# Kernel tuning notes

Hardware: AMD Instinct MI355X
Metric: run time of the kernel (lower is better)

## Reference

```python
import jax, jax.numpy as jnp
import numpy as np

HEAD_NUM = 16

def setup_inputs() -> dict:
    key = jax.random.key(0)
    kq, kk, kv = jax.random.split(key, 3)
    shape = (4, 2048, 1024)  # [B, N, C]
    return {
        "query_layer": jax.random.normal(kq, shape, dtype=jnp.float32),
        "key_layer": jax.random.normal(kk, shape, dtype=jnp.float32),
        "value_layer": jax.random.normal(kv, shape, dtype=jnp.float32),
    }

def _split_heads(x, h):
    B, N, C = x.shape
    return x.reshape(B, N, h, C // h).transpose(0, 2, 1, 3)  # [B,H,N,d]

def reference(query_layer, key_layer, value_layer):
    B, N, C = query_layer.shape
    h = HEAD_NUM
    d = C // h
    q = _split_heads(query_layer, h)
    k = _split_heads(key_layer, h)
    v = _split_heads(value_layer, h)
    scores = jnp.einsum('bhnd,bhmd->bhnm', q, k) / jnp.sqrt(jnp.asarray(d, q.dtype))
    probs = jax.nn.softmax(scores, axis=-1)
    ctx = jnp.einsum('bhnm,bhmd->bhnd', probs, v)
    return ctx.transpose(0, 2, 1, 3).reshape(B, N, C)
```

## Files before the change

### kernel.cpp

```cpp
#include <hip/hip_runtime.h>
#include <hip/hip_bf16.h>

#define B_   4
#define N_   2048
#define C_   1024
#define NT   32
#define QSCALE 0.18033688011112042f

typedef __attribute__((ext_vector_type(8)))  short short8;
typedef __attribute__((ext_vector_type(4)))  float f32x4;
typedef __attribute__((ext_vector_type(16))) float f32x16;
typedef __attribute__((ext_vector_type(2)))  int   int2v;

__device__ __forceinline__ unsigned short f2bf(float x) {
    union { __hip_bfloat16 h; unsigned short u; } c;
    c.h = __float2bfloat16(x);
    return c.u;
}
__device__ __forceinline__ float fast_exp2(float x) {
    float r; asm("v_exp_f32 %0, %1" : "=v"(r) : "v"(x)); return r;
}
__device__ __forceinline__ int cvtpk(float a, float b) {
    int r; asm("v_cvt_pk_bf16_f32 %0, %1, %2" : "=v"(r) : "v"(a), "v"(b)); return r;
}

__global__ __launch_bounds__(256) void prepack(
    const float* __restrict__ K, const float* __restrict__ V,
    unsigned short* __restrict__ Kt, unsigned short* __restrict__ Vt)
{
    __shared__ __align__(16) unsigned short kl[4096];
    __shared__ __align__(16) unsigned short vl[4096];
    const int L = blockIdx.x;
    const int xcd = L & 7;
    const int j = L >> 3;
    const int head = xcd + 8 * (j >> 5);
    const int t = j & 31;
    const int b = head >> 4, h = head & 15;
    const int tid = threadIdx.x;
    const int r = tid >> 2, cb = tid & 3;
    const size_t head_off = (size_t)b * N_ * C_ + (size_t)h * 64;
    const int kv0 = t * 64;
    const int blk_out = head * NT + t;

    {
        const float* src = K + head_off + (size_t)(kv0 + r) * C_ + cb * 16;
        f32x4 x0 = *(const f32x4*)(src);
        f32x4 x1 = *(const f32x4*)(src + 4);
        f32x4 x2 = *(const f32x4*)(src + 8);
        f32x4 x3 = *(const f32x4*)(src + 12);
        short8 p0, p1;
        #pragma unroll
        for (int i = 0; i < 4; ++i) {
            p0[i] = (short)f2bf(x0[i]); p0[i + 4] = (short)f2bf(x1[i]);
            p1[i] = (short)f2bf(x2[i]); p1[i + 4] = (short)f2bf(x3[i]);
        }
        const int swz = (r & 7) << 3;
        *(short8*)&kl[r * 64 + ((cb * 16) ^ swz)]     = p0;
        *(short8*)&kl[r * 64 + ((cb * 16 + 8) ^ swz)] = p1;
    }
    {
        const float* src = V + head_off + (size_t)(kv0 + r) * C_ + cb * 16;
        f32x4 y0 = *(const f32x4*)(src);
        f32x4 y1 = *(const f32x4*)(src + 4);
        f32x4 y2 = *(const f32x4*)(src + 8);
        f32x4 y3 = *(const f32x4*)(src + 12);
        #pragma unroll
        for (int i = 0; i < 4; ++i) {
            int d0 = cb * 16 + i;
            vl[d0 * 64 + (r ^ ((d0 & 7) << 3))] = f2bf(y0[i]);
            int d1 = cb * 16 + 4 + i;
            vl[d1 * 64 + (r ^ ((d1 & 7) << 3))] = f2bf(y1[i]);
            int d2 = cb * 16 + 8 + i;
            vl[d2 * 64 + (r ^ ((d2 & 7) << 3))] = f2bf(y2[i]);
            int d3 = cb * 16 + 12 + i;
            vl[d3 * 64 + (r ^ ((d3 & 7) << 3))] = f2bf(y3[i]);
        }
    }
    __syncthreads();
    #pragma unroll
    for (int cc = 0; cc < 2; ++cc) {
        const int c  = tid + cc * 256;
        const int f  = c >> 6;
        const int ln = c & 63;
        const int row = (f & 1) * 32 + (ln & 31);
        const int col = (f >> 1) * 16 + (ln >> 5) * 8;
        const int sw  = (row & 7) << 3;
        short8 kk = *(const short8*)&kl[row * 64 + (col ^ sw)];
        short8 vv = *(const short8*)&vl[row * 64 + (col ^ sw)];
        *(short8*)&Kt[(size_t)blk_out * 4096 + c * 8] = kk;
        *(short8*)&Vt[(size_t)blk_out * 4096 + c * 8] = vv;
    }
}

__global__ __launch_bounds__(256, 4) void attn_fwd(
    const float* __restrict__ Q, const unsigned short* __restrict__ Kt,
    const unsigned short* __restrict__ Vt, float* __restrict__ O)
{
    __shared__ __align__(16) unsigned short klds[2][4096];

    const int L = blockIdx.x;
    const int xcd = L & 7;
    const int j = L >> 3;
    const int head = xcd + 8 * (j >> 4);
    const int qt = j & 15;
    const int b = head >> 4, h = head & 15;

    const int tid  = threadIdx.x;
    const int wave = tid >> 6;
    const int lane = tid & 63;
    const int l31  = lane & 31;
    const int hi   = lane >> 5;

    const unsigned short* kbase = Kt + (size_t)head * (NT * 4096);
    const unsigned short* vbase = Vt + (size_t)head * (NT * 4096);
    const float* qp = Q + (size_t)b * N_ * C_ + (size_t)h * 64;
    float*       op = O + (size_t)b * N_ * C_ + (size_t)h * 64;

    const int qrow = qt * 128 + wave * 32 + l31;
    short8 qfrag[4];
    {
        const float* qr = qp + (size_t)qrow * C_ + hi * 8;
        #pragma unroll
        for (int ks = 0; ks < 4; ++ks) {
            f32x4 x0 = *(const f32x4*)(qr + ks * 16);
            f32x4 x1 = *(const f32x4*)(qr + ks * 16 + 4);
            short8 a;
            #pragma unroll
            for (int i = 0; i < 4; ++i) {
                a[i]     = (short)f2bf(x0[i] * QSCALE);
                a[i + 4] = (short)f2bf(x1[i] * QSCALE);
            }
            qfrag[ks] = a;
        }
    }

    f32x16 o0 = {}, o1 = {};
    float m_r = -3.0e38f, l_r = 0.0f;

    const int lofs = lane * 8;

    auto stageK = [&](int t, int buf) {
        const unsigned short* kg = kbase + (size_t)t * 4096 + wave * 1024 + lofs;
        __builtin_amdgcn_global_load_lds((const __attribute__((address_space(1))) void*)kg,
            (__attribute__((address_space(3))) void*)&klds[buf][wave * 1024], 16, 0, 0);
        __builtin_amdgcn_global_load_lds((const __attribute__((address_space(1))) void*)(kg + 512),
            (__attribute__((address_space(3))) void*)&klds[buf][wave * 1024 + 512], 16, 0, 0);
    };

    stageK(0, 0);
    __syncthreads();
    int cur = 0;

    for (int t = 0; t < NT; ++t) {
        if (t + 1 < NT) stageK(t + 1, cur ^ 1);

        const unsigned short* vtp = vbase + (size_t)t * 4096 + lofs;
        short8 vA0 = *(const short8*)(vtp);
        short8 vA1 = *(const short8*)(vtp + 512);
        short8 vA2 = *(const short8*)(vtp + 1024);
        short8 vA3 = *(const short8*)(vtp + 1536);

        const unsigned short* kl = klds[cur];

        f32x16 s0 = {}, s1 = {};
        __builtin_amdgcn_s_setprio(1);
        #pragma unroll
        for (int ks = 0; ks < 4; ++ks) {
            short8 kf0 = *(const short8*)&kl[ks * 1024 + lofs];
            short8 kf1 = *(const short8*)&kl[ks * 1024 + 512 + lofs];
            s0 = __builtin_amdgcn_mfma_f32_32x32x16_bf16(kf0, qfrag[ks], s0, 0, 0, 0);
            s1 = __builtin_amdgcn_mfma_f32_32x32x16_bf16(kf1, qfrag[ks], s1, 0, 0, 0);
        }
        __builtin_amdgcn_s_setprio(0);

        float mx[8];
        #pragma unroll
        for (int r = 0; r < 8; ++r) mx[r] = fmaxf(fmaxf(s0[r], s0[r + 8]), fmaxf(s1[r], s1[r + 8]));
        #pragma unroll
        for (int st = 4; st; st >>= 1) {
            #pragma unroll
            for (int r = 0; r < st; ++r) mx[r] = fmaxf(mx[r], mx[r + st]);
        }
        int2v msw = __builtin_amdgcn_permlane32_swap(__float_as_int(mx[0]), __float_as_int(mx[0]), false, false);
        const float rm = fmaxf(__int_as_float(msw[0]), __int_as_float(msw[1]));

        if (!__all(rm - m_r <= 8.0f)) {
            const float mnew = fmaxf(m_r, rm);
            const float corr = fast_exp2(m_r - mnew);
            m_r = mnew;
            l_r *= corr;
            #pragma unroll
            for (int r = 0; r < 16; ++r) { o0[r] *= corr; o1[r] *= corr; }
        }

        #pragma unroll
        for (int r = 0; r < 16; ++r) {
            s0[r] = fast_exp2(s0[r] - m_r);
            s1[r] = fast_exp2(s1[r] - m_r);
        }
        float aa[8];
        #pragma unroll
        for (int r = 0; r < 8; ++r) aa[r] = (s0[r] + s0[r + 8]) + (s1[r] + s1[r + 8]);
        #pragma unroll
        for (int st = 4; st; st >>= 1) {
            #pragma unroll
            for (int r = 0; r < st; ++r) aa[r] += aa[r + st];
        }
        int2v ssw = __builtin_amdgcn_permlane32_swap(__float_as_int(aa[0]), __float_as_int(aa[0]), false, false);
        l_r += __int_as_float(ssw[0]) + __int_as_float(ssw[1]);

        short8 pf[4];
        #pragma unroll
        for (int ct = 0; ct < 2; ++ct) {
            #pragma unroll
            for (int kss = 0; kss < 2; ++kss) {
                float e0, e1, e2, e3, e4, e5, e6, e7;
                if (ct == 0) {
                    e0 = s0[8*kss+0]; e1 = s0[8*kss+1]; e2 = s0[8*kss+2]; e3 = s0[8*kss+3];
                    e4 = s0[8*kss+4]; e5 = s0[8*kss+5]; e6 = s0[8*kss+6]; e7 = s0[8*kss+7];
                } else {
                    e0 = s1[8*kss+0]; e1 = s1[8*kss+1]; e2 = s1[8*kss+2]; e3 = s1[8*kss+3];
                    e4 = s1[8*kss+4]; e5 = s1[8*kss+5]; e6 = s1[8*kss+6]; e7 = s1[8*kss+7];
                }
                int w0 = cvtpk(e0, e1);
                int w1 = cvtpk(e2, e3);
                int w2 = cvtpk(e4, e5);
                int w3 = cvtpk(e6, e7);
                int2v sA = __builtin_amdgcn_permlane32_swap(w0, w2, false, false);
                int2v sB = __builtin_amdgcn_permlane32_swap(w1, w3, false, false);
                union { int i[4]; short8 v; } u;
                u.i[0] = sA[0]; u.i[1] = sB[0]; u.i[2] = sA[1]; u.i[3] = sB[1];
                pf[ct * 2 + kss] = u.v;
            }
        }

        short8 vB0 = *(const short8*)(vtp + 2048);
        short8 vB1 = *(const short8*)(vtp + 2560);
        short8 vB2 = *(const short8*)(vtp + 3072);
        short8 vB3 = *(const short8*)(vtp + 3584);

        __builtin_amdgcn_s_setprio(1);
        o0 = __builtin_amdgcn_mfma_f32_32x32x16_bf16(vA0, pf[0], o0, 0, 0, 0);
        o1 = __builtin_amdgcn_mfma_f32_32x32x16_bf16(vA1, pf[0], o1, 0, 0, 0);
        o0 = __builtin_amdgcn_mfma_f32_32x32x16_bf16(vA2, pf[1], o0, 0, 0, 0);
        o1 = __builtin_amdgcn_mfma_f32_32x32x16_bf16(vA3, pf[1], o1, 0, 0, 0);
        o0 = __builtin_amdgcn_mfma_f32_32x32x16_bf16(vB0, pf[2], o0, 0, 0, 0);
        o1 = __builtin_amdgcn_mfma_f32_32x32x16_bf16(vB1, pf[2], o1, 0, 0, 0);
        o0 = __builtin_amdgcn_mfma_f32_32x32x16_bf16(vB2, pf[3], o0, 0, 0, 0);
        o1 = __builtin_amdgcn_mfma_f32_32x32x16_bf16(vB3, pf[3], o1, 0, 0, 0);
        __builtin_amdgcn_s_setprio(0);

        __syncthreads();
        cur ^= 1;
    }

    const float inv = 1.0f / l_r;
    float* orow = op + (size_t)qrow * C_;
    #pragma unroll
    for (int bb = 0; bb < 4; ++bb) {
        f32x4 w0, w1;
        #pragma unroll
        for (int i = 0; i < 4; ++i) {
            w0[i] = o0[4 * bb + i] * inv;
            w1[i] = o1[4 * bb + i] * inv;
        }
        *(f32x4*)(orow + 8 * bb + 4 * hi)      = w0;
        *(f32x4*)(orow + 32 + 8 * bb + 4 * hi) = w1;
    }
}

extern "C" void kernel_launch(void* const* d_in, const int* in_sizes, int n_in,
                              void* d_out, int out_size, void* d_ws, size_t ws_size,
                              hipStream_t stream) {
    const float* q = (const float*)d_in[0];
    const float* k = (const float*)d_in[1];
    const float* v = (const float*)d_in[2];
    float* o = (float*)d_out;
    unsigned short* Kt = (unsigned short*)d_ws;
    unsigned short* Vt = Kt + (size_t)64 * NT * 4096;
    prepack<<<dim3(64 * NT), dim3(256), 0, stream>>>(k, v, Kt, Vt);
    attn_fwd<<<dim3(1024), dim3(256), 0, stream>>>(q, Kt, Vt, o);
}
```

Baseline: 113.7 us.

## Software-pipeline PV MFMA of previous tile with QK MFMA of current tile

Restructures the KV loop so the P·V matrix multiplies for tile t-1 are issued right after the Q·K multiplies for tile t. This interleaves the MFMA work with the softmax exp/convert work of the next tile, and double-buffers the probability fragments across iterations. It also folds the running-max subtraction into the score accumulator's initial value. The row-sum permlane reduction is deferred to a single swap at the end. The cost is more live registers (V fragments and two P buffers), which can lower occupancy or cause spills.

```diff
diff --git a/kernel.cpp b/kernel.cpp
--- a/kernel.cpp
+++ b/kernel.cpp
@@ -135,7 +135,7 @@
     }
 
     f32x16 o0 = {}, o1 = {};
-    float m_r = -3.0e38f, l_r = 0.0f;
+    float m_r = 0.0f, l_half = 0.0f;
 
     const int lofs = lane * 8;
 
@@ -147,22 +147,22 @@
             (__attribute__((address_space(3))) void*)&klds[buf][wave * 1024 + 512], 16, 0, 0);
     };
 
-    stageK(0, 0);
-    __syncthreads();
     int cur = 0;
-
-    for (int t = 0; t < NT; ++t) {
-        if (t + 1 < NT) stageK(t + 1, cur ^ 1);
-
-        const unsigned short* vtp = vbase + (size_t)t * 4096 + lofs;
-        short8 vA0 = *(const short8*)(vtp);
-        short8 vA1 = *(const short8*)(vtp + 512);
-        short8 vA2 = *(const short8*)(vtp + 1024);
-        short8 vA3 = *(const short8*)(vtp + 1536);
-
+    short8 pfA[4], pfB[4];
+    short8 vreg[8];
+
+    auto body = [&](int t, short8* pf_out, const short8* pf_in, bool first) {
         const unsigned short* kl = klds[cur];
 
-        f32x16 s0 = {}, s1 = {};
+        f32x16 s0, s1;
+        if (first) {
+            s0 = {}; s1 = {};
+        } else {
+            const float nm = -m_r;
+            #pragma unroll
+            for (int r = 0; r < 16; ++r) { s0[r] = nm; s1[r] = nm; }
+        }
+
         __builtin_amdgcn_s_setprio(1);
         #pragma unroll
         for (int ks = 0; ks < 4; ++ks) {
@@ -171,45 +171,66 @@
             s0 = __builtin_amdgcn_mfma_f32_32x32x16_bf16(kf0, qfrag[ks], s0, 0, 0, 0);
             s1 = __builtin_amdgcn_mfma_f32_32x32x16_bf16(kf1, qfrag[ks], s1, 0, 0, 0);
         }
+        if (!first) {
+            o0 = __builtin_amdgcn_mfma_f32_32x32x16_bf16(vreg[0], pf_in[0], o0, 0, 0, 0);
+            o1 = __builtin_amdgcn_mfma_f32_32x32x16_bf16(vreg[1], pf_in[0], o1, 0, 0, 0);
+            o0 = __builtin_amdgcn_mfma_f32_32x32x16_bf16(vreg[2], pf_in[1], o0, 0, 0, 0);
+            o1 = __builtin_amdgcn_mfma_f32_32x32x16_bf16(vreg[3], pf_in[1], o1, 0, 0, 0);
+            o0 = __builtin_amdgcn_mfma_f32_32x32x16_bf16(vreg[4], pf_in[2], o0, 0, 0, 0);
+            o1 = __builtin_amdgcn_mfma_f32_32x32x16_bf16(vreg[5], pf_in[2], o1, 0, 0, 0);
+            o0 = __builtin_amdgcn_mfma_f32_32x32x16_bf16(vreg[6], pf_in[3], o0, 0, 0, 0);
+            o1 = __builtin_amdgcn_mfma_f32_32x32x16_bf16(vreg[7], pf_in[3], o1, 0, 0, 0);
+        }
         __builtin_amdgcn_s_setprio(0);
 
+        if (t + 1 < NT) stageK(t + 1, cur ^ 1);
+
+        {
+            const unsigned short* vtp = vbase + (size_t)t * 4096 + lofs;
+            vreg[0] = *(const short8*)(vtp);
+            vreg[1] = *(const short8*)(vtp + 512);
+            vreg[2] = *(const short8*)(vtp + 1024);
+            vreg[3] = *(const short8*)(vtp + 1536);
+            vreg[4] = *(const short8*)(vtp + 2048);
+            vreg[5] = *(const short8*)(vtp + 2560);
+            vreg[6] = *(const short8*)(vtp + 3072);
+            vreg[7] = *(const short8*)(vtp + 3584);
+        }
+
         float mx[8];
         #pragma unroll
-        for (int r = 0; r < 8; ++r) mx[r] = fmaxf(fmaxf(s0[r], s0[r + 8]), fmaxf(s1[r], s1[r + 8]));
+        for (int r = 0; r < 8; ++r)
+            mx[r] = fmaxf(fmaxf(s0[r], s0[r + 8]), fmaxf(s1[r], s1[r + 8]));
         #pragma unroll
         for (int st = 4; st; st >>= 1) {
             #pragma unroll
             for (int r = 0; r < st; ++r) mx[r] = fmaxf(mx[r], mx[r + st]);
         }
         int2v msw = __builtin_amdgcn_permlane32_swap(__float_as_int(mx[0]), __float_as_int(mx[0]), false, false);
-        const float rm = fmaxf(__int_as_float(msw[0]), __int_as_float(msw[1]));
-
-        if (!__all(rm - m_r <= 8.0f)) {
-            const float mnew = fmaxf(m_r, rm);
-            const float corr = fast_exp2(m_r - mnew);
-            m_r = mnew;
-            l_r *= corr;
-            #pragma unroll
-            for (int r = 0; r < 16; ++r) { o0[r] *= corr; o1[r] *= corr; }
+        const float rmp = fmaxf(__int_as_float(msw[0]), __int_as_float(msw[1]));
+
+        if (first) {
+            m_r = rmp;
+            #pragma unroll
+            for (int r = 0; r < 16; ++r) { s0[r] -= rmp; s1[r] -= rmp; }
+        } else if (!__all(rmp <= 8.0f)) {
+            const float d = fmaxf(rmp, 0.0f);
+            const float corr = fast_exp2(-d);
+            m_r += d;
+            l_half *= corr;
+            #pragma unroll
+            for (int r = 0; r < 16; ++r) {
+                s0[r] -= d; s1[r] -= d;
+                o0[r] *= corr; o1[r] *= corr;
+            }
         }
 
         #pragma unroll
         for (int r = 0; r < 16; ++r) {
-            s0[r] = fast_exp2(s0[r] - m_r);
-            s1[r] = fast_exp2(s1[r] - m_r);
-        }
-        float aa[8];
-        #pragma unroll
-        for (int r = 0; r < 8; ++r) aa[r] = (s0[r] + s0[r + 8]) + (s1[r] + s1[r + 8]);
-        #pragma unroll
-        for (int st = 4; st; st >>= 1) {
-            #pragma unroll
-            for (int r = 0; r < st; ++r) aa[r] += aa[r + st];
-        }
-        int2v ssw = __builtin_amdgcn_permlane32_swap(__float_as_int(aa[0]), __float_as_int(aa[0]), false, false);
-        l_r += __int_as_float(ssw[0]) + __int_as_float(ssw[1]);
-
-        short8 pf[4];
+            s0[r] = fast_exp2(s0[r]);
+            s1[r] = fast_exp2(s1[r]);
+        }
+
         #pragma unroll
         for (int ct = 0; ct < 2; ++ct) {
             #pragma unroll
@@ -230,31 +251,49 @@
                 int2v sB = __builtin_amdgcn_permlane32_swap(w1, w3, false, false);
                 union { int i[4]; short8 v; } u;
                 u.i[0] = sA[0]; u.i[1] = sB[0]; u.i[2] = sA[1]; u.i[3] = sB[1];
-                pf[ct * 2 + kss] = u.v;
+                pf_out[ct * 2 + kss] = u.v;
             }
         }
 
-        short8 vB0 = *(const short8*)(vtp + 2048);
-        short8 vB1 = *(const short8*)(vtp + 2560);
-        short8 vB2 = *(const short8*)(vtp + 3072);
-        short8 vB3 = *(const short8*)(vtp + 3584);
-
-        __builtin_amdgcn_s_setprio(1);
-        o0 = __builtin_amdgcn_mfma_f32_32x32x16_bf16(vA0, pf[0], o0, 0, 0, 0);
-        o1 = __builtin_amdgcn_mfma_f32_32x32x16_bf16(vA1, pf[0], o1, 0, 0, 0);
-        o0 = __builtin_amdgcn_mfma_f32_32x32x16_bf16(vA2, pf[1], o0, 0, 0, 0);
-        o1 = __builtin_amdgcn_mfma_f32_32x32x16_bf16(vA3, pf[1], o1, 0, 0, 0);
-        o0 = __builtin_amdgcn_mfma_f32_32x32x16_bf16(vB0, pf[2], o0, 0, 0, 0);
-        o1 = __builtin_amdgcn_mfma_f32_32x32x16_bf16(vB1, pf[2], o1, 0, 0, 0);
-        o0 = __builtin_amdgcn_mfma_f32_32x32x16_bf16(vB2, pf[3], o0, 0, 0, 0);
-        o1 = __builtin_amdgcn_mfma_f32_32x32x16_bf16(vB3, pf[3], o1, 0, 0, 0);
-        __builtin_amdgcn_s_setprio(0);
+        float aa[8];
+        #pragma unroll
+        for (int r = 0; r < 8; ++r) aa[r] = (s0[r] + s0[r + 8]) + (s1[r] + s1[r + 8]);
+        #pragma unroll
+        for (int st = 4; st; st >>= 1) {
+            #pragma unroll
+            for (int r = 0; r < st; ++r) aa[r] += aa[r + st];
+        }
+        l_half += aa[0];
 
         __syncthreads();
         cur ^= 1;
-    }
-
+    };
+
+    stageK(0, 0);
+    __syncthreads();
+
+    body(0, pfA, pfB, true);
+    for (int t = 1; t < NT - 1; t += 2) {
+        body(t,     pfB, pfA, false);
+        body(t + 1, pfA, pfB, false);
+    }
+    body(NT - 1, pfB, pfA, false);
+
+    __builtin_amdgcn_s_setprio(1);
+    o0 = __builtin_amdgcn_mfma_f32_32x32x16_bf16(vreg[0], pfB[0], o0, 0, 0, 0);
+    o1 = __builtin_amdgcn_mfma_f32_32x32x16_bf16(vreg[1], pfB[0], o1, 0, 0, 0);
+    o0 = __builtin_amdgcn_mfma_f32_32x32x16_bf16(vreg[2], pfB[1], o0, 0, 0, 0);
+    o1 = __builtin_amdgcn_mfma_f32_32x32x16_bf16(vreg[3], pfB[1], o1, 0, 0, 0);
+    o0 = __builtin_amdgcn_mfma_f32_32x32x16_bf16(vreg[4], pfB[2], o0, 0, 0, 0);
+    o1 = __builtin_amdgcn_mfma_f32_32x32x16_bf16(vreg[5], pfB[2], o1, 0, 0, 0);
+    o0 = __builtin_amdgcn_mfma_f32_32x32x16_bf16(vreg[6], pfB[3], o0, 0, 0, 0);
+    o1 = __builtin_amdgcn_mfma_f32_32x32x16_bf16(vreg[7], pfB[3], o1, 0, 0, 0);
+    __builtin_amdgcn_s_setprio(0);
+
+    int2v lsw = __builtin_amdgcn_permlane32_swap(__float_as_int(l_half), __float_as_int(l_half), false, false);
+    const float l_r = __int_as_float(lsw[0]) + __int_as_float(lsw[1]);
     const float inv = 1.0f / l_r;
+
     float* orow = op + (size_t)qrow * C_;
     #pragma unroll
     for (int bb = 0; bb < 4; ++bb) {
```

Result: slower. 175.3 us (+54.1%).
